# Optimization experiments

Hardware: AMD Instinct MI355X
Metric: run time of the kernel (lower is better)

## Reference

```python
import jax, jax.numpy as jnp
import numpy as np

N_NODES = 100000
N_EDGES = 3200000
F_IN, HID, N_CLS = 256, 16, 40


def gcn_conv(x, row, col, W, b, n):
    """PyG GCNConv: x@W, symmetric deg^-1/2 normalization with self-loops, scatter-add to targets."""
    xw = x @ W  # [N, out]
    deg = jax.ops.segment_sum(jnp.ones_like(col, dtype=xw.dtype), col, num_segments=n)
    dinv = jnp.where(deg > 0, jax.lax.rsqrt(deg), jnp.zeros_like(deg))
    norm = dinv[row] * dinv[col]  # [E+N]
    out = jax.ops.segment_sum(norm[:, None] * xw[row], col, num_segments=n)
    return out + b


def setup_inputs() -> dict:
    key = jax.random.key(0)
    k1, k2, k3, k4 = jax.random.split(key, 4)
    x = jax.random.normal(k1, (N_NODES, F_IN), dtype=jnp.float32)
    edge_index = jax.random.randint(k2, (2, N_EDGES), 0, N_NODES, dtype=jnp.int64)
    W1 = jax.random.normal(k3, (F_IN, HID), dtype=jnp.float32) / np.sqrt(F_IN)
    b1 = jnp.zeros((HID,), dtype=jnp.float32)
    W2 = jax.random.normal(k4, (HID, N_CLS), dtype=jnp.float32) / np.sqrt(HID)
    b2 = jnp.zeros((N_CLS,), dtype=jnp.float32)
    return {"x": x, "edge_index": edge_index, "W1": W1, "b1": b1, "W2": W2, "b2": b2}


def reference(x, edge_index, W1, b1, W2, b2):
    n = x.shape[0]
    loop = jnp.arange(n, dtype=edge_index.dtype)
    row = jnp.concatenate([edge_index[0], loop])  # sources (+ self-loops)
    col = jnp.concatenate([edge_index[1], loop])  # targets (+ self-loops)
    h = gcn_conv(x, row, col, W1, b1, n)
    h = jax.nn.relu(h)
    # dropout p=0.5 is identity in eval mode (self.training == False)
    h = gcn_conv(h, row, col, W2, b2, n)
    return jax.nn.log_softmax(h, axis=1)
```

## Files before the change

### kernel.cpp

```cpp
#include <hip/hip_runtime.h>

#define F_IN 256
#define HID  16
#define NCLS 40
#define NB   512
#define CAP  18944
#define SPAN 4096

static inline int cdiv(int a, int b) { return (a + b - 1) / b; }

typedef short bf16x8 __attribute__((ext_vector_type(8)));
typedef float f32x4  __attribute__((ext_vector_type(4)));

__device__ __forceinline__ float bf_lo(unsigned int u) { return __uint_as_float(u << 16); }
__device__ __forceinline__ float bf_hi(unsigned int u) { return __uint_as_float(u & 0xFFFF0000u); }
__device__ __forceinline__ unsigned short f2bf(float a) {
    unsigned int u = __float_as_uint(a);
    return (unsigned short)((u + 0x7FFFu + ((u >> 16) & 1u)) >> 16);
}
__device__ __forceinline__ unsigned int pack_bf(float a, float b) {
    return (unsigned int)f2bf(a) | ((unsigned int)f2bf(b) << 16);
}

__global__ void __launch_bounds__(256) bcount_kernel(const int* __restrict__ col,
                                                     int* __restrict__ bkt_cnt, int E, int K) {
    __shared__ int h[256];
    int t = threadIdx.x;
    h[t] = 0;
    __syncthreads();
    int E4 = E >> 2;
    const int4* c4 = (const int4*)col;
    for (int e = blockIdx.x * 256 + t; e < E4; e += gridDim.x * 256) {
        int4 v = c4[e];
        atomicAdd(&h[v.x >> 9], 1);
        atomicAdd(&h[v.y >> 9], 1);
        atomicAdd(&h[v.z >> 9], 1);
        atomicAdd(&h[v.w >> 9], 1);
    }
    for (int e = (E4 << 2) + blockIdx.x * 256 + t; e < E; e += gridDim.x * 256)
        atomicAdd(&h[col[e] >> 9], 1);
    __syncthreads();
    if (t < K && h[t]) atomicAdd(&bkt_cnt[t], h[t]);
}

__global__ void __launch_bounds__(256) bscan_kernel(const int* __restrict__ bkt_cnt,
                                                    int* __restrict__ bkt_off,
                                                    int* __restrict__ bkt_cur, int K) {
    __shared__ int s[256];
    int t = threadIdx.x;
    int v = (t < K) ? bkt_cnt[t] : 0;
    s[t] = v;
    __syncthreads();
    for (int off = 1; off < 256; off <<= 1) {
        int x = (t >= off) ? s[t - off] : 0;
        __syncthreads();
        s[t] += x;
        __syncthreads();
    }
    int excl = s[t] - v;
    if (t < K) { bkt_off[t] = excl; bkt_cur[t] = excl; }
    if (t == K - 1) bkt_off[K] = excl + v;
}

__global__ void __launch_bounds__(256) bscatter_kernel(const int* __restrict__ row,
                                                       const int* __restrict__ col,
                                                       int* __restrict__ bkt_cur,
                                                       int* __restrict__ entries, int E) {
    __shared__ int cnt[256];
    __shared__ int base[256];
    int t = threadIdx.x;
    int start = blockIdx.x * SPAN;
    int end = min(start + SPAN, E);
    cnt[t] = 0;
    __syncthreads();
    int m = end - start;
    int m4 = m >> 2;
    const int4* c4 = (const int4*)(col + start);
    for (int i = t; i < m4; i += 256) {
        int4 v = c4[i];
        atomicAdd(&cnt[v.x >> 9], 1);
        atomicAdd(&cnt[v.y >> 9], 1);
        atomicAdd(&cnt[v.z >> 9], 1);
        atomicAdd(&cnt[v.w >> 9], 1);
    }
    for (int i = (m4 << 2) + t; i < m; i += 256)
        atomicAdd(&cnt[col[start + i] >> 9], 1);
    __syncthreads();
    int c = cnt[t];
    base[t] = c ? atomicAdd(&bkt_cur[t], c) : 0;
    cnt[t] = 0;
    __syncthreads();
    int e = start + t;
    for (; e + 768 < end; e += 1024) {
        int c0 = col[e];
        int c1 = col[e + 256];
        int c2 = col[e + 512];
        int c3 = col[e + 768];
        int r0 = row[e];
        int r1 = row[e + 256];
        int r2 = row[e + 512];
        int r3 = row[e + 768];
        int b0 = c0 >> 9, b1 = c1 >> 9, b2 = c2 >> 9, b3 = c3 >> 9;
        int p0 = base[b0] + atomicAdd(&cnt[b0], 1);
        int p1 = base[b1] + atomicAdd(&cnt[b1], 1);
        int p2 = base[b2] + atomicAdd(&cnt[b2], 1);
        int p3 = base[b3] + atomicAdd(&cnt[b3], 1);
        entries[p0] = r0 | ((c0 & (NB - 1)) << 17);
        entries[p1] = r1 | ((c1 & (NB - 1)) << 17);
        entries[p2] = r2 | ((c2 & (NB - 1)) << 17);
        entries[p3] = r3 | ((c3 & (NB - 1)) << 17);
    }
    for (; e < end; e += 256) {
        int cc = col[e];
        int bkt = cc >> 9;
        int pos = base[bkt] + atomicAdd(&cnt[bkt], 1);
        entries[pos] = row[e] | ((cc & (NB - 1)) << 17);
    }
}

__global__ void __launch_bounds__(512) bfill_kernel(const int* __restrict__ entries,
                                                    const int* __restrict__ bkt_off,
                                                    int* __restrict__ csr_src,
                                                    int* __restrict__ csr_off,
                                                    float* __restrict__ dinv, int n, int E) {
    __shared__ int sdeg[NB];
    __shared__ int soff[NB];
    __shared__ int wtot[8];
    __shared__ int lsrc[CAP];
    int t = threadIdx.x;
    int wv = t >> 6, ln = t & 63;
    int b = blockIdx.x;
    int node0 = b << 9;
    int nn = min(NB, n - node0);
    int seg0 = bkt_off[b], seg1 = bkt_off[b + 1];
    int m = seg1 - seg0;
    sdeg[t] = 0;
    __syncthreads();
    {
        int i = t;
        for (; i + 1536 < m; i += 2048) {
            int u0 = entries[seg0 + i];
            int u1 = entries[seg0 + i + 512];
            int u2 = entries[seg0 + i + 1024];
            int u3 = entries[seg0 + i + 1536];
            atomicAdd(&sdeg[u0 >> 17], 1);
            atomicAdd(&sdeg[u1 >> 17], 1);
            atomicAdd(&sdeg[u2 >> 17], 1);
            atomicAdd(&sdeg[u3 >> 17], 1);
        }
        for (; i < m; i += 512) atomicAdd(&sdeg[entries[seg0 + i] >> 17], 1);
    }
    __syncthreads();
    int v = sdeg[t];
    int inc = v;
#pragma unroll
    for (int o = 1; o < 64; o <<= 1) {
        int u = __shfl_up(inc, o);
        if (ln >= o) inc += u;
    }
    if (ln == 63) wtot[wv] = inc;
    __syncthreads();
    if (wv == 0) {
        int tv = (ln < 8) ? wtot[ln] : 0;
        int ti = tv;
#pragma unroll
        for (int o = 1; o < 8; o <<= 1) {
            int u = __shfl_up(ti, o);
            if (ln >= o) ti += u;
        }
        if (ln < 8) wtot[ln] = ti - tv;
    }
    __syncthreads();
    int excl = inc - v + wtot[wv];
    sdeg[t] = 0;
    soff[t] = excl;
    __syncthreads();
    {
        int i = t;
        for (; i + 1536 < m; i += 2048) {
            int u0 = entries[seg0 + i];
            int u1 = entries[seg0 + i + 512];
            int u2 = entries[seg0 + i + 1024];
            int u3 = entries[seg0 + i + 1536];
            int l0 = u0 >> 17, l1 = u1 >> 17, l2 = u2 >> 17, l3 = u3 >> 17;
            int p0 = soff[l0] + atomicAdd(&sdeg[l0], 1);
            int p1 = soff[l1] + atomicAdd(&sdeg[l1], 1);
            int p2 = soff[l2] + atomicAdd(&sdeg[l2], 1);
            int p3 = soff[l3] + atomicAdd(&sdeg[l3], 1);
            lsrc[p0] = u0 & 0x1FFFF;
            lsrc[p1] = u1 & 0x1FFFF;
            lsrc[p2] = u2 & 0x1FFFF;
            lsrc[p3] = u3 & 0x1FFFF;
        }
        for (; i < m; i += 512) {
            int u = entries[seg0 + i];
            int l = u >> 17;
            int pos = soff[l] + atomicAdd(&sdeg[l], 1);
            lsrc[pos] = u & 0x1FFFF;
        }
    }
    __syncthreads();
    for (int i = t; i < m; i += 512) csr_src[seg0 + i] = lsrc[i];
    if (t < nn) {
        csr_off[node0 + t] = seg0 + excl;
        dinv[node0 + t] = rsqrtf((float)(v + 1));
    }
    if (b == gridDim.x - 1 && t == 0) csr_off[n] = E;
}

__global__ void __launch_bounds__(256) xw_kernel(const float* __restrict__ x,
                                                 const float* __restrict__ W1,
                                                 const float* __restrict__ dinv,
                                                 unsigned short* __restrict__ f1,
                                                 int ntiles) {
    int lane = threadIdx.x & 63;
    int m = lane & 15;
    int q = lane >> 4;
    bf16x8 bfrag[8];
#pragma unroll
    for (int c = 0; c < 8; ++c) {
        const float* wp = W1 + (size_t)(c * 32 + q * 8) * HID + m;
#pragma unroll
        for (int j = 0; j < 8; ++j) bfrag[c][j] = (short)f2bf(wp[(size_t)j * HID]);
    }
    int wid = (blockIdx.x * 256 + threadIdx.x) >> 6;
    if (wid >= ntiles) return;
    int r0 = wid << 4;
    const float* xrow = x + (size_t)(r0 + m) * F_IN + q * 8;
    f32x4 acc = {0.f, 0.f, 0.f, 0.f};
#pragma unroll
    for (int c = 0; c < 8; ++c) {
        float4 v0 = *(const float4*)(xrow + c * 32);
        float4 v1 = *(const float4*)(xrow + c * 32 + 4);
        bf16x8 afrag;
        afrag[0] = (short)f2bf(v0.x);
        afrag[1] = (short)f2bf(v0.y);
        afrag[2] = (short)f2bf(v0.z);
        afrag[3] = (short)f2bf(v0.w);
        afrag[4] = (short)f2bf(v1.x);
        afrag[5] = (short)f2bf(v1.y);
        afrag[6] = (short)f2bf(v1.z);
        afrag[7] = (short)f2bf(v1.w);
        acc = __builtin_amdgcn_mfma_f32_16x16x32_bf16(afrag, bfrag[c], acc, 0, 0, 0);
    }
#pragma unroll
    for (int i = 0; i < 4; ++i) {
        int r = r0 + q * 4 + i;
        f1[(size_t)r * HID + m] = f2bf(dinv[r] * acc[i]);
    }
}

__global__ void __launch_bounds__(256) agg1_kernel(const uint2* __restrict__ feat2,
                                                   const float* __restrict__ dinv,
                                                   const int* __restrict__ csr_off,
                                                   const int* __restrict__ csr_src,
                                                   const float* __restrict__ b1,
                                                   uint2* __restrict__ f2, int n) {
    int wid = (blockIdx.x * 256 + threadIdx.x) >> 6;
    int w0 = wid << 1;
    if (w0 >= n) return;
    int lane = threadIdx.x & 63;
    int j = lane & 3;
    int s = (lane >> 2) & 7;
    int node = w0 + (lane >> 5);
    bool act = node < n;
    int start = 0, end = 0;
    if (act) { start = csr_off[node]; end = csr_off[node + 1]; }
    float a0 = 0.f, a1 = 0.f, a2 = 0.f, a3 = 0.f;
    for (int base = start + s; base < end; base += 32) {
        int e1 = base + 8, e2 = base + 16, e3 = base + 24;
        bool v1 = e1 < end, v2 = e2 < end, v3 = e3 < end;
        int i0 = csr_src[base];
        int i1 = csr_src[v1 ? e1 : base];
        int i2 = csr_src[v2 ? e2 : base];
        int i3 = csr_src[v3 ? e3 : base];
        uint2 u0 = feat2[(size_t)i0 * 4 + j];
        uint2 u1 = feat2[(size_t)i1 * 4 + j];
        uint2 u2 = feat2[(size_t)i2 * 4 + j];
        uint2 u3 = feat2[(size_t)i3 * 4 + j];
        if (!v1) { u1.x = 0u; u1.y = 0u; }
        if (!v2) { u2.x = 0u; u2.y = 0u; }
        if (!v3) { u3.x = 0u; u3.y = 0u; }
        a0 += bf_lo(u0.x); a1 += bf_hi(u0.x); a2 += bf_lo(u0.y); a3 += bf_hi(u0.y);
        a0 += bf_lo(u1.x); a1 += bf_hi(u1.x); a2 += bf_lo(u1.y); a3 += bf_hi(u1.y);
        a0 += bf_lo(u2.x); a1 += bf_hi(u2.x); a2 += bf_lo(u2.y); a3 += bf_hi(u2.y);
        a0 += bf_lo(u3.x); a1 += bf_hi(u3.x); a2 += bf_lo(u3.y); a3 += bf_hi(u3.y);
    }
    if (act && s == 0) {
        uint2 us = feat2[(size_t)node * 4 + j];
        a0 += bf_lo(us.x); a1 += bf_hi(us.x); a2 += bf_lo(us.y); a3 += bf_hi(us.y);
    }
    a0 += __shfl_xor(a0, 4);  a1 += __shfl_xor(a1, 4);  a2 += __shfl_xor(a2, 4);  a3 += __shfl_xor(a3, 4);
    a0 += __shfl_xor(a0, 8);  a1 += __shfl_xor(a1, 8);  a2 += __shfl_xor(a2, 8);  a3 += __shfl_xor(a3, 8);
    a0 += __shfl_xor(a0, 16); a1 += __shfl_xor(a1, 16); a2 += __shfl_xor(a2, 16); a3 += __shfl_xor(a3, 16);
    if ((lane & 31) < 4 && act) {
        float dc = dinv[node];
        float4 bb = *(const float4*)(b1 + 4 * j);
        float v0 = fmaxf(dc * a0 + bb.x, 0.f);
        float v1 = fmaxf(dc * a1 + bb.y, 0.f);
        float v2 = fmaxf(dc * a2 + bb.z, 0.f);
        float v3 = fmaxf(dc * a3 + bb.w, 0.f);
        uint2 o;
        o.x = pack_bf(dc * v0, dc * v1);
        o.y = pack_bf(dc * v2, dc * v3);
        f2[(size_t)node * 4 + j] = o;
    }
}

__global__ void __launch_bounds__(256) agg2out_kernel(const uint2* __restrict__ feat2,
                                                      const float* __restrict__ dinv,
                                                      const int* __restrict__ csr_off,
                                                      const int* __restrict__ csr_src,
                                                      const float* __restrict__ W2,
                                                      const float* __restrict__ b2,
                                                      float* __restrict__ out, int n) {
    __shared__ float W2s[HID * NCLS];
    __shared__ float b2s[NCLS];
    for (int i = threadIdx.x; i < HID * NCLS; i += 256) W2s[i] = W2[i];
    if (threadIdx.x < NCLS) b2s[threadIdx.x] = b2[threadIdx.x];
    __syncthreads();
    int wid = (blockIdx.x * 256 + threadIdx.x) >> 6;
    int w0 = wid << 1;
    if (w0 >= n) return;
    int lane = threadIdx.x & 63;
    int j = lane & 3;
    int s = (lane >> 2) & 7;
    int node = w0 + (lane >> 5);
    bool act = node < n;
    int start = 0, end = 0;
    if (act) { start = csr_off[node]; end = csr_off[node + 1]; }
    float a0 = 0.f, a1 = 0.f, a2 = 0.f, a3 = 0.f;
    for (int base = start + s; base < end; base += 32) {
        int e1 = base + 8, e2 = base + 16, e3 = base + 24;
        bool v1 = e1 < end, v2 = e2 < end, v3 = e3 < end;
        int i0 = csr_src[base];
        int i1 = csr_src[v1 ? e1 : base];
        int i2 = csr_src[v2 ? e2 : base];
        int i3 = csr_src[v3 ? e3 : base];
        uint2 u0 = feat2[(size_t)i0 * 4 + j];
        uint2 u1 = feat2[(size_t)i1 * 4 + j];
        uint2 u2 = feat2[(size_t)i2 * 4 + j];
        uint2 u3 = feat2[(size_t)i3 * 4 + j];
        if (!v1) { u1.x = 0u; u1.y = 0u; }
        if (!v2) { u2.x = 0u; u2.y = 0u; }
        if (!v3) { u3.x = 0u; u3.y = 0u; }
        a0 += bf_lo(u0.x); a1 += bf_hi(u0.x); a2 += bf_lo(u0.y); a3 += bf_hi(u0.y);
        a0 += bf_lo(u1.x); a1 += bf_hi(u1.x); a2 += bf_lo(u1.y); a3 += bf_hi(u1.y);
        a0 += bf_lo(u2.x); a1 += bf_hi(u2.x); a2 += bf_lo(u2.y); a3 += bf_hi(u2.y);
        a0 += bf_lo(u3.x); a1 += bf_hi(u3.x); a2 += bf_lo(u3.y); a3 += bf_hi(u3.y);
    }
    if (act && s == 0) {
        uint2 us = feat2[(size_t)node * 4 + j];
        a0 += bf_lo(us.x); a1 += bf_hi(us.x); a2 += bf_lo(us.y); a3 += bf_hi(us.y);
    }
    a0 += __shfl_xor(a0, 4);  a1 += __shfl_xor(a1, 4);  a2 += __shfl_xor(a2, 4);  a3 += __shfl_xor(a3, 4);
    a0 += __shfl_xor(a0, 8);  a1 += __shfl_xor(a1, 8);  a2 += __shfl_xor(a2, 8);  a3 += __shfl_xor(a3, 8);
    a0 += __shfl_xor(a0, 16); a1 += __shfl_xor(a1, 16); a2 += __shfl_xor(a2, 16); a3 += __shfl_xor(a3, 16);
    bool hasB = (w0 + 1) < n;
    float dcA = dinv[w0];
    float dcB = hasB ? dinv[w0 + 1] : 0.f;
    float zA = (lane < NCLS) ? b2s[lane] : 0.f;
    float zB = zA;
#pragma unroll
    for (int q = 0; q < 4; ++q) {
        float fA0 = dcA * __shfl(a0, q);
        float fA1 = dcA * __shfl(a1, q);
        float fA2 = dcA * __shfl(a2, q);
        float fA3 = dcA * __shfl(a3, q);
        float fB0 = dcB * __shfl(a0, 32 + q);
        float fB1 = dcB * __shfl(a1, 32 + q);
        float fB2 = dcB * __shfl(a2, 32 + q);
        float fB3 = dcB * __shfl(a3, 32 + q);
        if (lane < NCLS) {
            float w0v = W2s[(4 * q)     * NCLS + lane];
            float w1v = W2s[(4 * q + 1) * NCLS + lane];
            float w2v = W2s[(4 * q + 2) * NCLS + lane];
            float w3v = W2s[(4 * q + 3) * NCLS + lane];
            zA += fA0 * w0v + fA1 * w1v + fA2 * w2v + fA3 * w3v;
            zB += fB0 * w0v + fB1 * w1v + fB2 * w2v + fB3 * w3v;
        }
    }
    float mA = (lane < NCLS) ? zA : -INFINITY;
    float mB = (lane < NCLS) ? zB : -INFINITY;
#pragma unroll
    for (int off = 1; off < 64; off <<= 1) {
        mA = fmaxf(mA, __shfl_xor(mA, off));
        mB = fmaxf(mB, __shfl_xor(mB, off));
    }
    float eA = (lane < NCLS) ? __expf(zA - mA) : 0.f;
    float eB = (lane < NCLS) ? __expf(zB - mB) : 0.f;
#pragma unroll
    for (int off = 1; off < 64; off <<= 1) {
        eA += __shfl_xor(eA, off);
        eB += __shfl_xor(eB, off);
    }
    float lseA = mA + __logf(eA);
    float lseB = mB + __logf(eB);
    if (lane < NCLS) {
        out[(size_t)w0 * NCLS + lane] = zA - lseA;
        if (hasB) out[(size_t)(w0 + 1) * NCLS + lane] = zB - lseB;
    }
}

extern "C" void kernel_launch(void* const* d_in, const int* in_sizes, int n_in,
                              void* d_out, int out_size, void* d_ws, size_t ws_size,
                              hipStream_t stream) {
    const float* x   = (const float*)d_in[0];
    const int*   ei  = (const int*)d_in[1];
    const float* W1  = (const float*)d_in[2];
    const float* b1  = (const float*)d_in[3];
    const float* W2  = (const float*)d_in[4];
    const float* b2  = (const float*)d_in[5];
    float*       out = (float*)d_out;

    int n = in_sizes[0] / F_IN;
    int E = in_sizes[1] / 2;
    const int* rowp = ei;
    const int* colp = ei + E;
    int K = cdiv(n, NB);

    char* p = (char*)d_ws;
    auto alloc = [&](size_t bytes) {
        char* q = p;
        p += (bytes + 255) & ~(size_t)255;
        return q;
    };
    int*   bkt_cnt = (int*)  alloc((size_t)K * 4);
    int*   bkt_off = (int*)  alloc(((size_t)K + 1) * 4);
    int*   bkt_cur = (int*)  alloc((size_t)K * 4);
    int*   csr_off = (int*)  alloc(((size_t)n + 1) * 4);
    int*   csr_src = (int*)  alloc((size_t)E * 4);
    float* dinv    = (float*)alloc((size_t)n * 4);
    size_t fbytes = (size_t)n * HID * 2;
    char* region = alloc((size_t)E * 4 > 2 * fbytes ? (size_t)E * 4 : 2 * fbytes);
    int*            entries = (int*)region;
    unsigned short* f1      = (unsigned short*)region;
    uint2*          f2      = (uint2*)(region + fbytes);

    hipMemsetAsync(bkt_cnt, 0, (size_t)K * 4, stream);
    bcount_kernel<<<1024, 256, 0, stream>>>(colp, bkt_cnt, E, K);
    bscan_kernel<<<1, 256, 0, stream>>>(bkt_cnt, bkt_off, bkt_cur, K);
    bscatter_kernel<<<cdiv(E, SPAN), 256, 0, stream>>>(rowp, colp, bkt_cur, entries, E);
    bfill_kernel<<<K, 512, 0, stream>>>(entries, bkt_off, csr_src, csr_off, dinv, n, E);

    int ntiles = n >> 4;
    xw_kernel<<<cdiv(ntiles, 4), 256, 0, stream>>>(x, W1, dinv, f1, ntiles);
    int npair = cdiv(n, 2);
    agg1_kernel<<<cdiv(npair, 4), 256, 0, stream>>>((const uint2*)f1, dinv, csr_off, csr_src, b1, f2, n);
    agg2out_kernel<<<cdiv(npair, 4), 256, 0, stream>>>((const uint2*)f2, dinv, csr_off, csr_src, W2, b2, out, n);
}
```

Measured before the change: 337.5 us.

## Scatter CSR directly to global, widen bfill blocks, unroll scatter, prefetch self-loop

bfill drops its large LDS staging buffer and writes csr_src entries straight to global memory at their computed positions. It also runs with 1024 threads per block, which should raise occupancy because the big shared array is gone. bscatter's inner loop is unrolled from 4 to 8 edges per thread to keep more loads in flight, and both aggregation kernels issue the self-loop feature load before the edge loop. The trade-off is that global writes in bfill become scattered instead of coalesced, in exchange for no LDS capacity limit and more resident waves.

Result: slower. 348.2 us (+3.2%).

```diff
diff --git a/kernel.cpp b/kernel.cpp
--- a/kernel.cpp
+++ b/kernel.cpp
@@ -4,7 +4,6 @@
 #define HID  16
 #define NCLS 40
 #define NB   512
-#define CAP  18944
 #define SPAN 4096
 
 static inline int cdiv(int a, int b) { return (a + b - 1) / b; }
@@ -91,24 +90,41 @@
     cnt[t] = 0;
     __syncthreads();
     int e = start + t;
-    for (; e + 768 < end; e += 1024) {
+    for (; e + 1792 < end; e += 2048) {
         int c0 = col[e];
         int c1 = col[e + 256];
         int c2 = col[e + 512];
         int c3 = col[e + 768];
+        int c4v = col[e + 1024];
+        int c5 = col[e + 1280];
+        int c6 = col[e + 1536];
+        int c7 = col[e + 1792];
         int r0 = row[e];
         int r1 = row[e + 256];
         int r2 = row[e + 512];
         int r3 = row[e + 768];
+        int r4 = row[e + 1024];
+        int r5 = row[e + 1280];
+        int r6 = row[e + 1536];
+        int r7 = row[e + 1792];
         int b0 = c0 >> 9, b1 = c1 >> 9, b2 = c2 >> 9, b3 = c3 >> 9;
+        int b4 = c4v >> 9, b5 = c5 >> 9, b6 = c6 >> 9, b7 = c7 >> 9;
         int p0 = base[b0] + atomicAdd(&cnt[b0], 1);
         int p1 = base[b1] + atomicAdd(&cnt[b1], 1);
         int p2 = base[b2] + atomicAdd(&cnt[b2], 1);
         int p3 = base[b3] + atomicAdd(&cnt[b3], 1);
+        int p4 = base[b4] + atomicAdd(&cnt[b4], 1);
+        int p5 = base[b5] + atomicAdd(&cnt[b5], 1);
+        int p6 = base[b6] + atomicAdd(&cnt[b6], 1);
+        int p7 = base[b7] + atomicAdd(&cnt[b7], 1);
         entries[p0] = r0 | ((c0 & (NB - 1)) << 17);
         entries[p1] = r1 | ((c1 & (NB - 1)) << 17);
         entries[p2] = r2 | ((c2 & (NB - 1)) << 17);
         entries[p3] = r3 | ((c3 & (NB - 1)) << 17);
+        entries[p4] = r4 | ((c4v & (NB - 1)) << 17);
+        entries[p5] = r5 | ((c5 & (NB - 1)) << 17);
+        entries[p6] = r6 | ((c6 & (NB - 1)) << 17);
+        entries[p7] = r7 | ((c7 & (NB - 1)) << 17);
     }
     for (; e < end; e += 256) {
         int cc = col[e];
@@ -118,15 +134,14 @@
     }
 }
 
-__global__ void __launch_bounds__(512) bfill_kernel(const int* __restrict__ entries,
-                                                    const int* __restrict__ bkt_off,
-                                                    int* __restrict__ csr_src,
-                                                    int* __restrict__ csr_off,
-                                                    float* __restrict__ dinv, int n, int E) {
+__global__ void __launch_bounds__(1024) bfill_kernel(const int* __restrict__ entries,
+                                                     const int* __restrict__ bkt_off,
+                                                     int* __restrict__ csr_src,
+                                                     int* __restrict__ csr_off,
+                                                     float* __restrict__ dinv, int n, int E) {
     __shared__ int sdeg[NB];
     __shared__ int soff[NB];
     __shared__ int wtot[8];
-    __shared__ int lsrc[CAP];
     int t = threadIdx.x;
     int wv = t >> 6, ln = t & 63;
     int b = blockIdx.x;
@@ -134,31 +149,34 @@
     int nn = min(NB, n - node0);
     int seg0 = bkt_off[b], seg1 = bkt_off[b + 1];
     int m = seg1 - seg0;
-    sdeg[t] = 0;
+    if (t < NB) sdeg[t] = 0;
     __syncthreads();
     {
         int i = t;
-        for (; i + 1536 < m; i += 2048) {
+        for (; i + 3072 < m; i += 4096) {
             int u0 = entries[seg0 + i];
-            int u1 = entries[seg0 + i + 512];
-            int u2 = entries[seg0 + i + 1024];
-            int u3 = entries[seg0 + i + 1536];
+            int u1 = entries[seg0 + i + 1024];
+            int u2 = entries[seg0 + i + 2048];
+            int u3 = entries[seg0 + i + 3072];
             atomicAdd(&sdeg[u0 >> 17], 1);
             atomicAdd(&sdeg[u1 >> 17], 1);
             atomicAdd(&sdeg[u2 >> 17], 1);
             atomicAdd(&sdeg[u3 >> 17], 1);
         }
-        for (; i < m; i += 512) atomicAdd(&sdeg[entries[seg0 + i] >> 17], 1);
-    }
-    __syncthreads();
-    int v = sdeg[t];
-    int inc = v;
-#pragma unroll
-    for (int o = 1; o < 64; o <<= 1) {
-        int u = __shfl_up(inc, o);
-        if (ln >= o) inc += u;
-    }
-    if (ln == 63) wtot[wv] = inc;
+        for (; i < m; i += 1024) atomicAdd(&sdeg[entries[seg0 + i] >> 17], 1);
+    }
+    __syncthreads();
+    int v = 0, inc = 0;
+    if (t < NB) {
+        v = sdeg[t];
+        inc = v;
+#pragma unroll
+        for (int o = 1; o < 64; o <<= 1) {
+            int u = __shfl_up(inc, o);
+            if (ln >= o) inc += u;
+        }
+        if (ln == 63) wtot[wv] = inc;
+    }
     __syncthreads();
     if (wv == 0) {
         int tv = (ln < 8) ? wtot[ln] : 0;
@@ -171,41 +189,41 @@
         if (ln < 8) wtot[ln] = ti - tv;
     }
     __syncthreads();
-    int excl = inc - v + wtot[wv];
-    sdeg[t] = 0;
-    soff[t] = excl;
+    if (t < NB) {
+        int excl = inc - v + wtot[wv];
+        soff[t] = excl;
+        sdeg[t] = 0;
+        if (t < nn) {
+            csr_off[node0 + t] = seg0 + excl;
+            dinv[node0 + t] = rsqrtf((float)(v + 1));
+        }
+    }
+    if (b == gridDim.x - 1 && t == 0) csr_off[n] = E;
     __syncthreads();
     {
         int i = t;
-        for (; i + 1536 < m; i += 2048) {
+        for (; i + 3072 < m; i += 4096) {
             int u0 = entries[seg0 + i];
-            int u1 = entries[seg0 + i + 512];
-            int u2 = entries[seg0 + i + 1024];
-            int u3 = entries[seg0 + i + 1536];
+            int u1 = entries[seg0 + i + 1024];
+            int u2 = entries[seg0 + i + 2048];
+            int u3 = entries[seg0 + i + 3072];
             int l0 = u0 >> 17, l1 = u1 >> 17, l2 = u2 >> 17, l3 = u3 >> 17;
             int p0 = soff[l0] + atomicAdd(&sdeg[l0], 1);
             int p1 = soff[l1] + atomicAdd(&sdeg[l1], 1);
             int p2 = soff[l2] + atomicAdd(&sdeg[l2], 1);
             int p3 = soff[l3] + atomicAdd(&sdeg[l3], 1);
-            lsrc[p0] = u0 & 0x1FFFF;
-            lsrc[p1] = u1 & 0x1FFFF;
-            lsrc[p2] = u2 & 0x1FFFF;
-            lsrc[p3] = u3 & 0x1FFFF;
-        }
-        for (; i < m; i += 512) {
+            csr_src[seg0 + p0] = u0 & 0x1FFFF;
+            csr_src[seg0 + p1] = u1 & 0x1FFFF;
+            csr_src[seg0 + p2] = u2 & 0x1FFFF;
+            csr_src[seg0 + p3] = u3 & 0x1FFFF;
+        }
+        for (; i < m; i += 1024) {
             int u = entries[seg0 + i];
             int l = u >> 17;
             int pos = soff[l] + atomicAdd(&sdeg[l], 1);
-            lsrc[pos] = u & 0x1FFFF;
-        }
-    }
-    __syncthreads();
-    for (int i = t; i < m; i += 512) csr_src[seg0 + i] = lsrc[i];
-    if (t < nn) {
-        csr_off[node0 + t] = seg0 + excl;
-        dinv[node0 + t] = rsqrtf((float)(v + 1));
-    }
-    if (b == gridDim.x - 1 && t == 0) csr_off[n] = E;
+            csr_src[seg0 + pos] = u & 0x1FFFF;
+        }
+    }
 }
 
 __global__ void __launch_bounds__(256) xw_kernel(const float* __restrict__ x,
@@ -266,6 +284,8 @@
     bool act = node < n;
     int start = 0, end = 0;
     if (act) { start = csr_off[node]; end = csr_off[node + 1]; }
+    bool sl = act && (s == 0);
+    uint2 us = feat2[(size_t)(act ? node : 0) * 4 + j];
     float a0 = 0.f, a1 = 0.f, a2 = 0.f, a3 = 0.f;
     for (int base = start + s; base < end; base += 32) {
         int e1 = base + 8, e2 = base + 16, e3 = base + 24;
@@ -286,8 +306,7 @@
         a0 += bf_lo(u2.x); a1 += bf_hi(u2.x); a2 += bf_lo(u2.y); a3 += bf_hi(u2.y);
         a0 += bf_lo(u3.x); a1 += bf_hi(u3.x); a2 += bf_lo(u3.y); a3 += bf_hi(u3.y);
     }
-    if (act && s == 0) {
-        uint2 us = feat2[(size_t)node * 4 + j];
+    if (sl) {
         a0 += bf_lo(us.x); a1 += bf_hi(us.x); a2 += bf_lo(us.y); a3 += bf_hi(us.y);
     }
     a0 += __shfl_xor(a0, 4);  a1 += __shfl_xor(a1, 4);  a2 += __shfl_xor(a2, 4);  a3 += __shfl_xor(a3, 4);
@@ -329,6 +348,8 @@
     bool act = node < n;
     int start = 0, end = 0;
     if (act) { start = csr_off[node]; end = csr_off[node + 1]; }
+    bool sl = act && (s == 0);
+    uint2 us = feat2[(size_t)(act ? node : 0) * 4 + j];
     float a0 = 0.f, a1 = 0.f, a2 = 0.f, a3 = 0.f;
     for (int base = start + s; base < end; base += 32) {
         int e1 = base + 8, e2 = base + 16, e3 = base + 24;
@@ -349,8 +370,7 @@
         a0 += bf_lo(u2.x); a1 += bf_hi(u2.x); a2 += bf_lo(u2.y); a3 += bf_hi(u2.y);
         a0 += bf_lo(u3.x); a1 += bf_hi(u3.x); a2 += bf_lo(u3.y); a3 += bf_hi(u3.y);
     }
-    if (act && s == 0) {
-        uint2 us = feat2[(size_t)node * 4 + j];
+    if (sl) {
         a0 += bf_lo(us.x); a1 += bf_hi(us.x); a2 += bf_lo(us.y); a3 += bf_hi(us.y);
     }
     a0 += __shfl_xor(a0, 4);  a1 += __shfl_xor(a1, 4);  a2 += __shfl_xor(a2, 4);  a3 += __shfl_xor(a3, 4);
@@ -441,7 +461,7 @@
     bcount_kernel<<<1024, 256, 0, stream>>>(colp, bkt_cnt, E, K);
     bscan_kernel<<<1, 256, 0, stream>>>(bkt_cnt, bkt_off, bkt_cur, K);
     bscatter_kernel<<<cdiv(E, SPAN), 256, 0, stream>>>(rowp, colp, bkt_cur, entries, E);
-    bfill_kernel<<<K, 512, 0, stream>>>(entries, bkt_off, csr_src, csr_off, dinv, n, E);
+    bfill_kernel<<<K, 1024, 0, stream>>>(entries, bkt_off, csr_src, csr_off, dinv, n, E);
 
     int ntiles = n >> 4;
     xw_kernel<<<cdiv(ntiles, 4), 256, 0, stream>>>(x, W1, dinv, f1, ntiles);
```
